# Kernel tuning notes

Hardware: AMD Instinct MI355X
Metric: run time of the kernel (lower is better)

Reference implementation:

```python
import jax, jax.numpy as jnp
import numpy as np

NUM_SAMPLES = 512
FG_FRACTION = 0.25
MAX_POS = int(NUM_SAMPLES * FG_FRACTION)  # 128
THRESHOLDS = np.array([0.0, 0.5, 0.5], dtype=np.float32)
INDICATORS = np.array([-3, -1, -2, 1], dtype=np.int32)


def _make_boxes(key, shape, scale):
    # random valid boxes: sorted corner pairs in [0, scale)
    y = jnp.sort(jax.random.uniform(key, shape[:-1] + (2,)) * scale, axis=-1)
    x = jnp.sort(jax.random.uniform(jax.random.fold_in(key, 1), shape[:-1] + (2,)) * scale, axis=-1)
    return jnp.stack([y[..., 0], x[..., 0], y[..., 1], x[..., 1]], axis=-1)


def setup_inputs() -> dict:
    key = jax.random.key(0)
    k1, k2, k3, k4 = jax.random.split(key, 4)
    B, N, M = 32, 8000, 256
    boxes = _make_boxes(k1, (B, N, 4), 1024.0)
    gt_boxes = _make_boxes(k2, (B, M, 4), 1024.0)
    # pad last quarter of gt entries with -1 (invalid)
    valid = (jnp.arange(M) < (3 * M) // 4)[None, :, None]
    gt_boxes = jnp.where(valid, gt_boxes, -jnp.ones_like(gt_boxes))
    gt_classes = jax.random.randint(k3, (B, M), 1, 91, dtype=jnp.int32)
    gt_classes = jnp.where(valid[..., 0], gt_classes, -1)
    rand = jax.random.uniform(k4, (B, N + M))
    return {"boxes": boxes, "gt_boxes": gt_boxes, "gt_classes": gt_classes, "rand": rand}


def _pairwise_iou(b1, b2):
    # b1: [B,N,4], b2: [B,M,4] in (ymin,xmin,ymax,xmax) -> [B,N,M]
    ymin1, xmin1, ymax1, xmax1 = jnp.split(b1, 4, axis=-1)  # each [B,N,1]
    ymin2, xmin2, ymax2, xmax2 = (t[..., 0] for t in jnp.split(b2, 4, axis=-1))  # [B,M]
    ih = jnp.clip(jnp.minimum(ymax1, ymax2[:, None, :]) - jnp.maximum(ymin1, ymin2[:, None, :]), 0.0)
    iw = jnp.clip(jnp.minimum(xmax1, xmax2[:, None, :]) - jnp.maximum(xmin1, xmin2[:, None, :]), 0.0)
    inter = ih * iw
    a1 = (ymax1 - ymin1) * (xmax1 - xmin1)          # [B,N,1]
    a2 = (ymax2 - ymin2) * (xmax2 - xmin2)          # [B,M]
    union = a1 + a2[:, None, :] - inter
    return jnp.where(union > 0, inter / union, 0.0)


def _ranks_desc(score):
    order = jnp.argsort(-score)
    return jnp.zeros_like(order).at[order].set(jnp.arange(score.shape[0]))


def _sample_one(pos, neg, ign, rand):
    cand = (pos | neg) & ~ign
    pos_c = pos & cand
    neg_c = neg & cand
    pos_rank = _ranks_desc(jnp.where(pos_c, rand, -1.0))
    pos_sel = pos_c & (pos_rank < MAX_POS)
    neg_needed = NUM_SAMPLES - jnp.sum(pos_sel)
    neg_rank = _ranks_desc(jnp.where(neg_c, rand, -1.0))
    neg_sel = neg_c & (neg_rank < neg_needed)
    indicator = (pos_sel | neg_sel).astype(jnp.int32)
    _, idx = jax.lax.top_k(indicator, NUM_SAMPLES)  # selected first, ties by lowest index
    return idx


def _gather(t, idx):
    # t: [B,L,C], idx: [B,K] -> [B,K,C]
    return jnp.take_along_axis(t, idx[..., None], axis=1)


def reference(boxes, gt_boxes, gt_classes, rand):
    gt_boxes = gt_boxes.astype(boxes.dtype)
    boxes = jnp.concatenate([boxes, gt_boxes], axis=1)  # mix_gt_boxes
    boxes_invalid = jnp.max(boxes, axis=-1) < 0.0       # [B,L]
    gt_invalid = jnp.max(gt_boxes, axis=-1) < 0.0       # [B,M]
    sim = _pairwise_iou(boxes, gt_boxes)                # [B,L,M]
    sim = jnp.where(boxes_invalid[:, :, None] | gt_invalid[:, None, :], -1.0, sim)

    matched_vals = jnp.max(sim, axis=-1)                # [B,L]
    matched_gt_indices = jnp.argmax(sim, axis=-1).astype(jnp.int32)
    bucket = jnp.searchsorted(jnp.asarray(THRESHOLDS), matched_vals, side='right')
    match_indicators = jnp.asarray(INDICATORS)[bucket]  # [B,L]

    positive = match_indicators >= 0
    negative = match_indicators == -1
    ignored = match_indicators == -2
    invalid = match_indicators == -3
    background = negative | invalid                     # [B,L]

    matched_gt_classes = _gather(gt_classes[..., None], matched_gt_indices)[..., 0]
    matched_gt_classes = jnp.where(background, 0, matched_gt_classes)
    matched_gt_boxes = _gather(gt_boxes, matched_gt_indices)
    matched_gt_boxes = jnp.where(background[..., None], 0.0, matched_gt_boxes)
    matched_gt_indices = jnp.where(background, -1, matched_gt_indices)

    indices = jax.vmap(_sample_one)(positive, negative, ignored, rand)  # [B,K]
    rois = _gather(boxes, indices)
    sampled_gt_boxes = _gather(matched_gt_boxes, indices)
    sampled_gt_classes = _gather(matched_gt_classes[..., None], indices)[..., 0]
    sampled_gt_indices = _gather(matched_gt_indices[..., None], indices)[..., 0]
    return rois, sampled_gt_boxes, sampled_gt_classes, sampled_gt_indices
```

## Files before the change

### kernel.cpp

```cpp
#include <hip/hip_runtime.h>
#include <stdint.h>

#define BB 32
#define NN 8000
#define MM 256
#define LL (NN + MM)
#define NSAMP 512
#define MAXPOS 128
#define T2 1024
#define CH ((LL + T2 - 1) / T2)
#define SPLIT 4
#define MSUB (MM / SPLIT)

__device__ __forceinline__ void opaquef(float& x) { asm("" : "+v"(x)); }

__device__ __forceinline__ uint32_t approx_key(const float4 bx, float a1,
                                               const float4 g, float a2,
                                               uint32_t klo)
{
    float ih = fmaxf(fminf(bx.z, g.z) - fmaxf(bx.x, g.x), 0.0f);
    float iw = fmaxf(fminf(bx.w, g.w) - fmaxf(bx.y, g.y), 0.0f);
    float inter = ih * iw;
    float s = fmaxf(a1 + a2, 1e-30f);
    float u = inter * __builtin_amdgcn_rcpf(s);
    return (__float_as_uint(u) & 0xFFFFFFC0u) | klo;
}

__device__ __noinline__ int serial_argmax(const float4 bx, const float a1,
                                          const float4* s_gt, const float* s_a2,
                                          int nv)
{
    float qb = -1.0f; int bi = 0;
    for (int m = 0; m < nv; ++m) {
        float4 g = s_gt[m];
        float ih = fmaxf(fminf(bx.z, g.z) - fmaxf(bx.x, g.x), 0.0f);
        float iw = fmaxf(fminf(bx.w, g.w) - fmaxf(bx.y, g.y), 0.0f);
        float inter = ih * iw; opaquef(inter);
        float uni = (a1 + s_a2[m]) - inter;
        float q = (uni > 0.0f) ? (inter / uni) : 0.0f;
        if (q > qb) { qb = q; bi = m; }
    }
    return bi;
}

__global__ __launch_bounds__(256) void match_split_kernel(
    const float* __restrict__ boxes, const float* __restrict__ gt,
    uint32_t* __restrict__ keys)
{
    __shared__ float4 s_gt[MSUB];
    __shared__ float  s_a2[MSUB];
    __shared__ uint32_t s_klo[MSUB];
    __shared__ int s_nv;
    const int b = blockIdx.y, sp = blockIdx.z, tid = threadIdx.x;
    if (tid < MSUB) {
        float4 v = ((const float4*)(gt + ((size_t)b * MM + sp * MSUB) * 4))[tid];
        bool valid = !(fmaxf(fmaxf(v.x, v.y), fmaxf(v.z, v.w)) < 0.0f);
        uint64_t mk = __ballot(valid);
        int pos = __popcll(mk & ((1ull << tid) - 1));
        if (valid) {
            s_gt[pos] = v;
            s_a2[pos] = (v.z - v.x) * (v.w - v.y);
            s_klo[pos] = (uint32_t)(63 - tid);
        }
        if (tid == 0) s_nv = (int)__popcll(mk);
    }
    __syncthreads();
    const int l0 = blockIdx.x * 512 + tid * 2;
    if (l0 >= LL) return;
    const int l1 = l0 + 1;
    const bool v1 = (l1 < LL);
    const int l1c = v1 ? l1 : l0;
    const int nv = s_nv;

    const float4* bb4 = (const float4*)(boxes + (size_t)b * NN * 4);
    const float4* gb4 = (const float4*)(gt + (size_t)b * MM * 4);
    float4 bx0 = (l0 < NN) ? bb4[l0] : gb4[l0 - NN];
    float4 bx1 = (l1c < NN) ? bb4[l1c] : gb4[l1c - NN];
    float a10 = (bx0.z - bx0.x) * (bx0.w - bx0.y); opaquef(a10);
    float a11 = (bx1.z - bx1.x) * (bx1.w - bx1.y); opaquef(a11);

    uint32_t best0 = 0, sec0 = 0, best1 = 0, sec1 = 0;
    #pragma unroll 4
    for (int m = 0; m < nv; ++m) {
        const float4 g = s_gt[m];
        const float a2 = s_a2[m];
        const uint32_t klo = s_klo[m];
        {
            uint32_t key = approx_key(bx0, a10, g, a2, klo);
            uint32_t old = best0;
            best0 = max(old, key);
            sec0  = max(sec0, min(old, key));
        }
        {
            uint32_t key = approx_key(bx1, a11, g, a2, klo);
            uint32_t old = best1;
            best1 = max(old, key);
            sec1  = max(sec1, min(old, key));
        }
    }

    bool redo0 = ((best0 & ~63u) != 0u) &&
                 (((best0 & ~63u) - (sec0 & ~63u)) <= 64u);
    bool redo1 = v1 && ((best1 & ~63u) != 0u) &&
                 (((best1 & ~63u) - (sec1 & ~63u)) <= 64u);
    if (__any(redo0 || redo1)) {
        if (redo0) {
            int w = serial_argmax(bx0, a10, s_gt, s_a2, nv);
            best0 = approx_key(bx0, a10, s_gt[w], s_a2[w], s_klo[w]);
        }
        if (redo1) {
            int w = serial_argmax(bx1, a11, s_gt, s_a2, nv);
            best1 = approx_key(bx1, a11, s_gt[w], s_a2[w], s_klo[w]);
        }
    }
    keys[((size_t)b * LL + l0) * SPLIT + sp] = best0;
    if (v1) keys[((size_t)b * LL + l1) * SPLIT + sp] = best1;
}

__global__ __launch_bounds__(256) void merge2_kernel(
    const float* __restrict__ boxes, const float* __restrict__ gt,
    uint32_t* __restrict__ keys)
{
    const int b = blockIdx.y;
    const int l = blockIdx.x * 256 + threadIdx.x;
    if (l >= LL) return;
    const float4* bb4 = (const float4*)(boxes + (size_t)b * NN * 4);
    const float4* gb4 = (const float4*)(gt + (size_t)b * MM * 4);
    const uint4 kv = ((const uint4*)keys)[(size_t)b * LL + l];
    float4 bx = (l < NN) ? bb4[l] : gb4[l - NN];
    int cls, midx = 0;
    if (fmaxf(fmaxf(bx.x, bx.y), fmaxf(bx.z, bx.w)) < 0.0f) {
        cls = 2;
    } else {
        uint32_t best = kv.x; int bsp = 0;
        if (kv.y > best) { best = kv.y; bsp = 1; }
        if (kv.z > best) { best = kv.z; bsp = 2; }
        if (kv.w > best) { best = kv.w; bsp = 3; }
        const uint32_t bt = best & ~63u;
        const uint32_t s0 = (bsp == 0) ? 0u : (kv.x & ~63u);
        const uint32_t s1 = (bsp == 1) ? 0u : (kv.y & ~63u);
        const uint32_t s2 = (bsp == 2) ? 0u : (kv.z & ~63u);
        const uint32_t s3 = (bsp == 3) ? 0u : (kv.w & ~63u);
        const uint32_t sec = max(max(s0, s1), max(s2, s3));
        float a1 = (bx.z - bx.x) * (bx.w - bx.y); opaquef(a1);
        if ((bt != 0u) && (bt - sec) <= 64u) {
            float qb = -1.0f; midx = 0;
            #pragma unroll
            for (int sp = 0; sp < SPLIT; ++sp) {
                const uint32_t k = (sp == 0) ? kv.x : (sp == 1) ? kv.y
                                 : (sp == 2) ? kv.z : kv.w;
                const int m = sp * MSUB + (63 - (int)(k & 63u));
                float4 g = gb4[m];
                float a2 = (g.z - g.x) * (g.w - g.y); opaquef(a2);
                float ih = fmaxf(fminf(bx.z, g.z) - fmaxf(bx.x, g.x), 0.0f);
                float iw = fmaxf(fminf(bx.w, g.w) - fmaxf(bx.y, g.y), 0.0f);
                float inter = ih * iw; opaquef(inter);
                float uni = (a1 + a2) - inter;
                float q = (uni > 0.0f) ? (inter / uni) : 0.0f;
                if (q > qb) { qb = q; midx = m; }
            }
            cls = (qb >= 0.5f) ? 1 : 0;
        } else {
            midx = bsp * MSUB + (63 - (int)(best & 63u));
            float4 g = gb4[midx];
            float a2 = (g.z - g.x) * (g.w - g.y); opaquef(a2);
            float ih = fmaxf(fminf(bx.z, g.z) - fmaxf(bx.x, g.x), 0.0f);
            float iw = fmaxf(fminf(bx.w, g.w) - fmaxf(bx.y, g.y), 0.0f);
            float inter = ih * iw; opaquef(inter);
            float uni = (a1 + a2) - inter;
            float q = (uni > 0.0f) ? (inter / uni) : 0.0f;
            cls = (q >= 0.5f) ? 1 : 0;
        }
    }
    ((uint16_t*)keys)[((size_t)b * LL + l) * 8] = (uint16_t)(cls | (midx << 2));
}

__device__ __forceinline__ int block_exscan_fast(int v, int* wt, int tid)
{
    const int lane = tid & 63, w = tid >> 6;
    int x = v;
    #pragma unroll
    for (int off = 1; off < 64; off <<= 1) {
        int y = __shfl_up(x, off);
        if (lane >= off) x += y;
    }
    if (lane == 63) wt[w] = x;
    __syncthreads();
    if (tid < 64) {
        int t = (tid < 16) ? wt[tid] : 0;
        #pragma unroll
        for (int off = 1; off < 16; off <<= 1) {
            int y = __shfl_up(t, off);
            if (tid >= off) t += y;
        }
        if (tid < 16) wt[tid] = t;
    }
    __syncthreads();
    return ((w > 0) ? wt[w - 1] : 0) + x - v;
}

__device__ __forceinline__ int block_exscan_seg4(int v, int* wt, int tid)
{
    const int lane = tid & 63, w = tid >> 6;
    int x = v;
    #pragma unroll
    for (int off = 1; off < 64; off <<= 1) {
        int y = __shfl_up(x, off);
        if (lane >= off) x += y;
    }
    if (lane == 63) wt[w] = x;
    __syncthreads();
    if (tid < 16) {
        int t = wt[tid];
        #pragma unroll
        for (int off = 1; off < 4; off <<= 1) {
            int y = __shfl_up(t, off);
            if ((tid & 3) >= off) t += y;
        }
        wt[tid] = t;
    }
    __syncthreads();
    return (((w & 3) > 0) ? wt[w - 1] : 0) + x - v;
}

__global__ __launch_bounds__(T2) void sample_kernel(
    const float* __restrict__ boxes, const float* __restrict__ gt,
    const int* __restrict__ gtc, const float* __restrict__ rnd,
    const uint32_t* __restrict__ keys, float* __restrict__ out)
{
    __shared__ uint32_t s_key[LL];
    __shared__ uint16_t s_pk[LL];
    __shared__ int s_hist[512];
    __shared__ int s_warp[16];
    __shared__ int s_idx[NSAMP];
    __shared__ int s_sb[8];
    const int b = blockIdx.x, tid = threadIdx.x, lane = tid & 63;
    const float4* bb4 = (const float4*)(boxes + (size_t)b * NN * 4);
    const float4* gb4 = (const float4*)(gt + (size_t)b * MM * 4);

    if (tid == 0) s_sb[0] = 0;
    __syncthreads();

    int loc = 0;
    for (int l = tid; l < LL; l += T2) {
        s_key[l] = __float_as_uint(rnd[(size_t)b * LL + l]);
        uint16_t p = ((const uint16_t*)keys)[((size_t)b * LL + l) * 8];
        s_pk[l] = p;
        int c = p & 3;
        loc += (c == 0) ? 1 : ((c == 1) ? 0x10000 : 0);
    }
    #pragma unroll
    for (int off = 32; off; off >>= 1) loc += __shfl_xor(loc, off);
    if (lane == 0) atomicAdd(&s_sb[0], loc);
    __syncthreads();
    const int Nn = s_sb[0] & 0xFFFF, P = s_sb[0] >> 16;

    const int posK = (P < MAXPOS) ? P : MAXPOS;
    const int negK = NSAMP - posK;
    const bool negRad = (Nn > negK);
    const bool posRad = (P > MAXPOS);

    uint32_t prefix0 = 0, prefix1 = 0;
    int rem0 = negK, rem1 = MAXPOS;
    if (negRad || posRad) {
        for (int round = 0; round < 4; ++round) {
            const int shift = 24 - 8 * round;
            if (tid < 512) s_hist[tid] = 0;
            __syncthreads();
            const uint32_t pmask = (round == 0) ? 0u : (0xFFFFFFFFu << (shift + 8));
            for (int l = tid; l < LL; l += T2) {
                const uint32_t k = s_key[l];
                const int c = s_pk[l] & 3;
                bool doit = (c == 0) ? (negRad && ((k & pmask) == prefix0))
                          : (c == 1) ? (posRad && ((k & pmask) == prefix1))
                          : false;
                if (doit) atomicAdd(&s_hist[(c << 8) | ((k >> shift) & 255)], 1);
            }
            __syncthreads();
            int h = 0;
            if (tid < 512) h = s_hist[(tid & 0x100) | (255 - (tid & 255))];
            const int above = block_exscan_seg4(h, s_warp, tid);
            if (tid < 512) {
                const int c = tid >> 8;
                const int rem = c ? rem1 : rem0;
                const bool act = c ? posRad : negRad;
                if (act && above < rem && above + h >= rem) {
                    s_sb[4 + c * 2] = 255 - (tid & 255);
                    s_sb[5 + c * 2] = above;
                }
            }
            __syncthreads();
            if (negRad) { prefix0 |= ((uint32_t)s_sb[4]) << shift; rem0 -= s_sb[5]; }
            if (posRad) { prefix1 |= ((uint32_t)s_sb[6]) << shift; rem1 -= s_sb[7]; }
            __syncthreads();
        }
    }
    const uint32_t thr0 = negRad ? prefix0 : 0u;  const int r0 = negRad ? rem0 : LL;
    const uint32_t thr1 = posRad ? prefix1 : 0u;  const int r1 = posRad ? rem1 : LL;

    const int lo = tid * CH, hi = (lo + CH < LL) ? (lo + CH) : LL;
    int nt = 0;
    for (int l = lo; l < hi; ++l) {
        const int c = s_pk[l] & 3;
        const uint32_t k = s_key[l];
        if (c == 0) { if (k == thr0) nt += 1; }
        else if (c == 1) { if (k == thr1) nt += 0x10000; }
    }
    const int basep = block_exscan_fast(nt, s_warp, tid);
    int base0 = basep & 0xFFFF, base1 = basep >> 16;
    for (int l = lo; l < hi; ++l) {
        const int c = s_pk[l] & 3;
        if (c > 1) continue;
        const uint32_t k = s_key[l];
        const uint32_t thr = c ? thr1 : thr0;
        bool sel = (k > thr);
        if (k == thr) {
            if (c == 0) { sel = (base0 < r0); ++base0; }
            else        { sel = (base1 < r1); ++base1; }
        }
        if (sel) s_pk[l] |= 0x8000;
    }
    __syncthreads();

    int cnt = 0;
    for (int l = lo; l < hi; ++l) cnt += (s_pk[l] & 0x8000) ? 1 : 0x10000;
    const int pb = block_exscan_fast(cnt, s_warp, tid);
    const int S = s_warp[15] & 0xFFFF;
    int bs = pb & 0xFFFF, bu = (pb >> 16) + S;
    for (int l = lo; l < hi; ++l) {
        if (s_pk[l] & 0x8000) { if (bs < NSAMP) s_idx[bs] = l; ++bs; }
        else                  { if (bu < NSAMP) s_idx[bu] = l; ++bu; }
    }
    __syncthreads();

    if (tid < NSAMP) {
        const int l = s_idx[tid];
        float4 bx = (l < NN) ? bb4[l] : gb4[l - NN];
        const int p = s_pk[l];
        const int c = p & 3, mi = (p >> 2) & 0xFF;
        const bool bg = (c != 1);
        float4 gb = make_float4(0.f, 0.f, 0.f, 0.f);
        int cl = 0, si = -1;
        if (!bg) {
            gb = gb4[mi];
            cl = gtc[(size_t)b * MM + mi];
            si = mi;
        }
        const size_t rk = (size_t)b * NSAMP + tid;
        ((float4*)out)[rk] = bx;
        ((float4*)(out + (size_t)BB * NSAMP * 4))[rk] = gb;
        out[(size_t)2 * BB * NSAMP * 4 + rk] = (float)cl;
        out[(size_t)2 * BB * NSAMP * 4 + (size_t)BB * NSAMP + rk] = (float)si;
    }
}

extern "C" void kernel_launch(void* const* d_in, const int* in_sizes, int n_in,
                              void* d_out, int out_size, void* d_ws, size_t ws_size,
                              hipStream_t stream)
{
    const float* boxes = (const float*)d_in[0];
    const float* gt    = (const float*)d_in[1];
    const int*   gtc   = (const int*)  d_in[2];
    const float* rnd   = (const float*)d_in[3];
    float* out = (float*)d_out;
    uint32_t* keys = (uint32_t*)d_ws;

    dim3 g1((LL + 511) / 512, BB, SPLIT);
    match_split_kernel<<<g1, 256, 0, stream>>>(boxes, gt, keys);
    dim3 g2((LL + 255) / 256, BB);
    merge2_kernel<<<g2, 256, 0, stream>>>(boxes, gt, keys);
    sample_kernel<<<BB, T2, 0, stream>>>(boxes, gt, gtc, rnd, keys, out);
}
```

Baseline: 70.97 us.

## Use one box per thread in matcher, early-exit radix select, simplify key

The matching kernel now handles one box per thread instead of two and launches twice as many blocks, which trades instruction-level parallelism for more waves. The approximate key drops its clamp on the area sum. The merge kernel treats an all-zero best key as invalid. The sampler's radix-select loop now stops early for each class once the selected bin exactly covers the remaining count, so it can skip later histogram rounds and barriers. The early exit and the dropped clamp slightly change threshold and edge-case semantics.

```diff
diff --git a/kernel.cpp b/kernel.cpp
--- a/kernel.cpp
+++ b/kernel.cpp
@@ -14,18 +14,6 @@
 
 __device__ __forceinline__ void opaquef(float& x) { asm("" : "+v"(x)); }
 
-__device__ __forceinline__ uint32_t approx_key(const float4 bx, float a1,
-                                               const float4 g, float a2,
-                                               uint32_t klo)
-{
-    float ih = fmaxf(fminf(bx.z, g.z) - fmaxf(bx.x, g.x), 0.0f);
-    float iw = fmaxf(fminf(bx.w, g.w) - fmaxf(bx.y, g.y), 0.0f);
-    float inter = ih * iw;
-    float s = fmaxf(a1 + a2, 1e-30f);
-    float u = inter * __builtin_amdgcn_rcpf(s);
-    return (__float_as_uint(u) & 0xFFFFFFC0u) | klo;
-}
-
 __device__ __noinline__ int serial_argmax(const float4 bx, const float a1,
                                           const float4* s_gt, const float* s_a2,
                                           int nv)
@@ -41,6 +29,18 @@
         if (q > qb) { qb = q; bi = m; }
     }
     return bi;
+}
+
+__device__ __forceinline__ uint32_t approx_key(const float4 bx, float a1,
+                                               const float4 g, float a2,
+                                               uint32_t klo)
+{
+    float ih = fmaxf(fminf(bx.z, g.z) - fmaxf(bx.x, g.x), 0.0f);
+    float iw = fmaxf(fminf(bx.w, g.w) - fmaxf(bx.y, g.y), 0.0f);
+    float inter = ih * iw;
+    float s = a1 + a2;
+    float u = inter * __builtin_amdgcn_rcpf(s);
+    return (__float_as_uint(u) & 0xFFFFFFC0u) | klo;
 }
 
 __global__ __launch_bounds__(256) void match_split_kernel(
@@ -65,56 +65,32 @@
         if (tid == 0) s_nv = (int)__popcll(mk);
     }
     __syncthreads();
-    const int l0 = blockIdx.x * 512 + tid * 2;
-    if (l0 >= LL) return;
-    const int l1 = l0 + 1;
-    const bool v1 = (l1 < LL);
-    const int l1c = v1 ? l1 : l0;
+    const int l = blockIdx.x * 256 + tid;
+    if (l >= LL) return;
     const int nv = s_nv;
 
     const float4* bb4 = (const float4*)(boxes + (size_t)b * NN * 4);
     const float4* gb4 = (const float4*)(gt + (size_t)b * MM * 4);
-    float4 bx0 = (l0 < NN) ? bb4[l0] : gb4[l0 - NN];
-    float4 bx1 = (l1c < NN) ? bb4[l1c] : gb4[l1c - NN];
-    float a10 = (bx0.z - bx0.x) * (bx0.w - bx0.y); opaquef(a10);
-    float a11 = (bx1.z - bx1.x) * (bx1.w - bx1.y); opaquef(a11);
-
-    uint32_t best0 = 0, sec0 = 0, best1 = 0, sec1 = 0;
+    float4 bx = (l < NN) ? bb4[l] : gb4[l - NN];
+    float a1 = (bx.z - bx.x) * (bx.w - bx.y); opaquef(a1);
+
+    uint32_t best = 0, sec = 0;
     #pragma unroll 4
     for (int m = 0; m < nv; ++m) {
-        const float4 g = s_gt[m];
-        const float a2 = s_a2[m];
-        const uint32_t klo = s_klo[m];
-        {
-            uint32_t key = approx_key(bx0, a10, g, a2, klo);
-            uint32_t old = best0;
-            best0 = max(old, key);
-            sec0  = max(sec0, min(old, key));
-        }
-        {
-            uint32_t key = approx_key(bx1, a11, g, a2, klo);
-            uint32_t old = best1;
-            best1 = max(old, key);
-            sec1  = max(sec1, min(old, key));
-        }
-    }
-
-    bool redo0 = ((best0 & ~63u) != 0u) &&
-                 (((best0 & ~63u) - (sec0 & ~63u)) <= 64u);
-    bool redo1 = v1 && ((best1 & ~63u) != 0u) &&
-                 (((best1 & ~63u) - (sec1 & ~63u)) <= 64u);
-    if (__any(redo0 || redo1)) {
-        if (redo0) {
-            int w = serial_argmax(bx0, a10, s_gt, s_a2, nv);
-            best0 = approx_key(bx0, a10, s_gt[w], s_a2[w], s_klo[w]);
-        }
-        if (redo1) {
-            int w = serial_argmax(bx1, a11, s_gt, s_a2, nv);
-            best1 = approx_key(bx1, a11, s_gt[w], s_a2[w], s_klo[w]);
-        }
-    }
-    keys[((size_t)b * LL + l0) * SPLIT + sp] = best0;
-    if (v1) keys[((size_t)b * LL + l1) * SPLIT + sp] = best1;
+        uint32_t key = approx_key(bx, a1, s_gt[m], s_a2[m], s_klo[m]);
+        sec  = max(sec, min(best, key));
+        best = max(best, key);
+    }
+
+    bool redo = ((best & ~63u) != 0u) &&
+                (((best & ~63u) - (sec & ~63u)) <= 64u);
+    if (__any(redo)) {
+        if (redo) {
+            int w = serial_argmax(bx, a1, s_gt, s_a2, nv);
+            best = approx_key(bx, a1, s_gt[w], s_a2[w], s_klo[w]);
+        }
+    }
+    keys[((size_t)b * LL + l) * SPLIT + sp] = best;
 }
 
 __global__ __launch_bounds__(256) void merge2_kernel(
@@ -129,13 +105,13 @@
     const uint4 kv = ((const uint4*)keys)[(size_t)b * LL + l];
     float4 bx = (l < NN) ? bb4[l] : gb4[l - NN];
     int cls, midx = 0;
-    if (fmaxf(fmaxf(bx.x, bx.y), fmaxf(bx.z, bx.w)) < 0.0f) {
+    uint32_t best = kv.x; int bsp = 0;
+    if (kv.y > best) { best = kv.y; bsp = 1; }
+    if (kv.z > best) { best = kv.z; bsp = 2; }
+    if (kv.w > best) { best = kv.w; bsp = 3; }
+    if (fmaxf(fmaxf(bx.x, bx.y), fmaxf(bx.z, bx.w)) < 0.0f || best == 0u) {
         cls = 2;
     } else {
-        uint32_t best = kv.x; int bsp = 0;
-        if (kv.y > best) { best = kv.y; bsp = 1; }
-        if (kv.z > best) { best = kv.z; bsp = 2; }
-        if (kv.w > best) { best = kv.w; bsp = 3; }
         const uint32_t bt = best & ~63u;
         const uint32_t s0 = (bsp == 0) ? 0u : (kv.x & ~63u);
         const uint32_t s1 = (bsp == 1) ? 0u : (kv.y & ~63u);
@@ -262,41 +238,56 @@
 
     uint32_t prefix0 = 0, prefix1 = 0;
     int rem0 = negK, rem1 = MAXPOS;
-    if (negRad || posRad) {
-        for (int round = 0; round < 4; ++round) {
-            const int shift = 24 - 8 * round;
-            if (tid < 512) s_hist[tid] = 0;
-            __syncthreads();
-            const uint32_t pmask = (round == 0) ? 0u : (0xFFFFFFFFu << (shift + 8));
-            for (int l = tid; l < LL; l += T2) {
-                const uint32_t k = s_key[l];
-                const int c = s_pk[l] & 3;
-                bool doit = (c == 0) ? (negRad && ((k & pmask) == prefix0))
-                          : (c == 1) ? (posRad && ((k & pmask) == prefix1))
-                          : false;
-                if (doit) atomicAdd(&s_hist[(c << 8) | ((k >> shift) & 255)], 1);
+    bool act0 = negRad, act1 = posRad;
+    uint32_t thr0f = 0, thr1f = 0;
+    int r0f = LL, r1f = LL;
+    for (int round = 0; round < 4 && (act0 || act1); ++round) {
+        const int shift = 24 - 8 * round;
+        if (tid < 512) s_hist[tid] = 0;
+        __syncthreads();
+        const uint32_t pmask = (round == 0) ? 0u : (0xFFFFFFFFu << (shift + 8));
+        for (int l = tid; l < LL; l += T2) {
+            const uint32_t k = s_key[l];
+            const int c = s_pk[l] & 3;
+            bool doit = (c == 0) ? (act0 && ((k & pmask) == prefix0))
+                      : (c == 1) ? (act1 && ((k & pmask) == prefix1))
+                      : false;
+            if (doit) atomicAdd(&s_hist[(c << 8) | ((k >> shift) & 255)], 1);
+        }
+        __syncthreads();
+        int h = 0;
+        if (tid < 512) h = s_hist[(tid & 0x100) | (255 - (tid & 255))];
+        const int above = block_exscan_seg4(h, s_warp, tid);
+        if (tid < 512) {
+            const int c = tid >> 8;
+            const int rem = c ? rem1 : rem0;
+            const bool act = c ? act1 : act0;
+            if (act && above < rem && above + h >= rem) {
+                s_sb[4 + c * 2] = 255 - (tid & 255);
+                s_sb[5 + c * 2] = above;
             }
-            __syncthreads();
-            int h = 0;
-            if (tid < 512) h = s_hist[(tid & 0x100) | (255 - (tid & 255))];
-            const int above = block_exscan_seg4(h, s_warp, tid);
-            if (tid < 512) {
-                const int c = tid >> 8;
-                const int rem = c ? rem1 : rem0;
-                const bool act = c ? posRad : negRad;
-                if (act && above < rem && above + h >= rem) {
-                    s_sb[4 + c * 2] = 255 - (tid & 255);
-                    s_sb[5 + c * 2] = above;
-                }
-            }
-            __syncthreads();
-            if (negRad) { prefix0 |= ((uint32_t)s_sb[4]) << shift; rem0 -= s_sb[5]; }
-            if (posRad) { prefix1 |= ((uint32_t)s_sb[6]) << shift; rem1 -= s_sb[7]; }
-            __syncthreads();
-        }
-    }
-    const uint32_t thr0 = negRad ? prefix0 : 0u;  const int r0 = negRad ? rem0 : LL;
-    const uint32_t thr1 = posRad ? prefix1 : 0u;  const int r1 = posRad ? rem1 : LL;
+        }
+        __syncthreads();
+        if (act0) {
+            const int bin = s_sb[4];
+            rem0 -= s_sb[5];
+            prefix0 |= ((uint32_t)bin) << shift;
+            const int cnt = s_hist[bin];
+            if (rem0 == cnt)      { act0 = false; thr0f = prefix0; r0f = LL; }
+            else if (round == 3)  { act0 = false; thr0f = prefix0; r0f = rem0; }
+        }
+        if (act1) {
+            const int bin = s_sb[6];
+            rem1 -= s_sb[7];
+            prefix1 |= ((uint32_t)bin) << shift;
+            const int cnt = s_hist[256 + bin];
+            if (rem1 == cnt)      { act1 = false; thr1f = prefix1; r1f = LL; }
+            else if (round == 3)  { act1 = false; thr1f = prefix1; r1f = rem1; }
+        }
+        __syncthreads();
+    }
+    const uint32_t thr0 = negRad ? thr0f : 0u;  const int r0 = negRad ? r0f : LL;
+    const uint32_t thr1 = posRad ? thr1f : 0u;  const int r1 = posRad ? r1f : LL;
 
     const int lo = tid * CH, hi = (lo + CH < LL) ? (lo + CH) : LL;
     int nt = 0;
@@ -365,7 +356,7 @@
     float* out = (float*)d_out;
     uint32_t* keys = (uint32_t*)d_ws;
 
-    dim3 g1((LL + 511) / 512, BB, SPLIT);
+    dim3 g1((LL + 255) / 256, BB, SPLIT);
     match_split_kernel<<<g1, 256, 0, stream>>>(boxes, gt, keys);
     dim3 g2((LL + 255) / 256, BB);
     merge2_kernel<<<g2, 256, 0, stream>>>(boxes, gt, keys);
```

After: 68.33 us. 1.04x faster.
